# Kernel optimization log

Measured on AMD Instinct MI355X. Metric: run time of the kernel, lower is better.

## Reference

```python
import jax, jax.numpy as jnp
import numpy as np

TOPK, NUM_CLASSES = 13, 80
ALPHA, BETA, GAMMA, EPS = 1.0, 5.0, 3.0, 1e-09


def _make_boxes(key, shape, img=640.0, wmin=10.0, wmax=120.0):
    k1, k2 = jax.random.split(key)
    cxy = jax.random.uniform(k1, shape[:-1] + (2,), minval=0.0, maxval=img)
    wh = jax.random.uniform(k2, shape[:-1] + (2,), minval=wmin, maxval=wmax)
    return jnp.concatenate([cxy - wh / 2, cxy + wh / 2], axis=-1)


def setup_inputs() -> dict:
    key = jax.random.key(0)
    ks = jax.random.split(key, 7)
    bs, A, C, n = 16, 8400, 80, 60
    return {
        'pd_scores': jax.random.uniform(ks[0], (bs, A, C), dtype=jnp.float32),
        'pd_bboxes': _make_boxes(ks[1], (bs, A, 4)),
        'pd_angles': jax.random.uniform(ks[2], (bs, A, 1), minval=0.0, maxval=90.0),
        'anc_points': jax.random.uniform(ks[3], (A, 2), minval=0.0, maxval=640.0),
        'gt_labels': jax.random.randint(ks[4], (bs, n, 1), 0, C, dtype=jnp.int32),
        'gt_bboxes': _make_boxes(ks[5], (bs, n, 4)),
        'gt_angles': jax.random.uniform(ks[6], (bs, n, 1), minval=0.0, maxval=90.0),
        'mask_gt': jnp.ones((bs, n, 1), jnp.float32),
        'epoch_num': 1,
    }


def _cos_fn(x, ar, beta=2.0):
    return 0.5 + 0.5 * jnp.cos(beta / ar * x / 180.0 * jnp.pi + jnp.pi * (1.0 - beta / (2.0 * ar)))


def _angle_measure(pd_angles, gt_angles, gt_bboxes):
    # gt area ratio w/h -> (bs, n, 1, 1)
    w = gt_bboxes[..., 2:3] - gt_bboxes[..., 0:1]
    h = gt_bboxes[..., 3:4] - gt_bboxes[..., 1:2]
    ar = (w / (h + 1e-05))[:, :, None, :]
    theta = jnp.abs(gt_angles[:, :, None, :] - pd_angles[:, None, :, :])  # (bs,n,A,1)
    av = 1.0 / ar / (2.0 - 1.0 / ar)
    mx = _cos_fn(0.0, ar)
    mn = _cos_fn(90.0, ar)
    r = (_cos_fn(theta, ar) - mn) / (mx - mn) * (1.0 - av) + av
    r = jnp.where(jnp.isnan(r), 0.0, r)
    return jnp.squeeze(r, -1)  # (bs, n, A)


def _pairwise_iou(gt, pd):
    # gt (bs,n,4), pd (bs,A,4) -> (bs,n,A)
    lt = jnp.maximum(gt[:, :, None, :2], pd[:, None, :, :2])
    rb = jnp.minimum(gt[:, :, None, 2:], pd[:, None, :, 2:])
    inter = jnp.clip(rb - lt, 0.0).prod(-1)
    a1 = jnp.clip(gt[..., 2:] - gt[..., :2], 0.0).prod(-1)[:, :, None]
    a2 = jnp.clip(pd[..., 2:] - pd[..., :2], 0.0).prod(-1)[:, None, :]
    return inter / (a1 + a2 - inter + EPS)


def _select_topk(metrics, topk_mask):
    bs, n, A = metrics.shape
    _, idxs = jax.lax.top_k(metrics, TOPK)
    idxs = jnp.where(topk_mask, idxs, 0)
    flat = idxs.reshape(bs * n, TOPK)
    cnt = jnp.zeros((bs * n, A), jnp.int32).at[jnp.arange(bs * n)[:, None], flat].add(1)
    cnt = cnt.reshape(bs, n, A)
    return jnp.where(cnt > 1, 0, cnt).astype(metrics.dtype)


def _select_highest_overlaps(mask_pos, overlaps, n):
    fg = mask_pos.sum(-2)                                   # (bs, A)
    multi = fg[:, None, :] > 1                              # (bs, 1, A)
    is_max = jax.nn.one_hot(overlaps.argmax(1), n, axis=1, dtype=mask_pos.dtype)  # (bs,n,A)
    mask_pos = jnp.where(multi, is_max, mask_pos)
    fg = mask_pos.sum(-2)
    tgt_idx = mask_pos.argmax(-2)                           # (bs, A)
    return tgt_idx, fg, mask_pos


def reference(pd_scores, pd_bboxes, pd_angles, anc_points, gt_labels, gt_bboxes, gt_angles, mask_gt, epoch_num):
    bs, A, C = pd_scores.shape
    n = gt_bboxes.shape[1]
    lab = gt_labels[..., 0].astype(jnp.int32)               # (bs, n)

    # bbox_scores: pd_scores[b, :, gt_label] -> (bs, n, A)
    pts = jnp.transpose(pd_scores, (0, 2, 1))               # (bs, C, A)
    bbox_scores = jnp.take_along_axis(pts, lab[:, :, None], axis=1)

    overlaps = _pairwise_iou(gt_bboxes, pd_bboxes)          # (bs, n, A)
    ang = _angle_measure(pd_angles, gt_angles, gt_bboxes)   # (bs, n, A)
    align = bbox_scores ** ALPHA * overlaps ** BETA * ang ** GAMMA

    # anchors-inside-gt mask (bs, n, A)
    lt = anc_points[None, None, :, :] - gt_bboxes[:, :, None, :2]
    rb = gt_bboxes[:, :, None, 2:] - anc_points[None, None, :, :]
    in_gts = (jnp.concatenate([lt, rb], -1).min(-1) > EPS).astype(align.dtype)

    topk_mask = jnp.broadcast_to(mask_gt > 0, (bs, n, TOPK))
    mask_topk = _select_topk(align * in_gts, topk_mask)
    mask_pos = mask_topk * in_gts * mask_gt                 # (bs, n, A)

    tgt_idx, fg, mask_pos = _select_highest_overlaps(mask_pos, overlaps, n)

    # gather per-anchor targets from flattened gt tensors
    off = tgt_idx + jnp.arange(bs, dtype=tgt_idx.dtype)[:, None] * n   # (bs, A)
    tlab = lab.reshape(-1)[off]
    tlab = jnp.where(tlab < 0, 0, tlab)
    tbb = gt_bboxes.reshape(-1, 4)[off]                     # (bs, A, 4)
    tang = gt_angles.reshape(-1, 1)[off]                    # (bs, A, 1)
    ts = jax.nn.one_hot(tlab, C, dtype=pd_scores.dtype)     # (bs, A, C)
    ts = jnp.where(fg[:, :, None] > 0, ts, 0.0)

    # normalized alignment metric scaling
    align = align * mask_pos
    pam = align.max(-1, keepdims=True)                      # (bs, n, 1)
    pov = (overlaps * mask_pos).max(-1, keepdims=True)      # (bs, n, 1)
    norm = (align * pov / (pam + EPS)).max(-2)[:, :, None]  # (bs, A, 1)
    ts = ts * norm

    return tlab, tbb, tang, ts, fg > 0
```

## Files before the change

### kernel.cpp

```cpp
#include <hip/hip_runtime.h>
#include <math.h>

#define TOPK 13
#define PI_F 3.14159265358979323846f
#define RPB 4
#define NC 4
#define CAP 64

typedef unsigned int u32;
typedef unsigned long long u64;

__device__ __forceinline__ u32 ford(float f) {
    u32 u = __float_as_uint(f);
    return (u & 0x80000000u) ? ~u : (u | 0x80000000u);
}
__device__ __forceinline__ float funord(u32 o) {
    u32 u = (o & 0x80000000u) ? (o & 0x7FFFFFFFu) : ~o;
    return __uint_as_float(u);
}

__device__ __forceinline__ float iou_fn(float4 g, float4 p) {
    float ltx = fmaxf(g.x, p.x), lty = fmaxf(g.y, p.y);
    float rbx = fminf(g.z, p.z), rby = fminf(g.w, p.w);
    float inter = fmaxf(rbx - ltx, 0.0f) * fmaxf(rby - lty, 0.0f);
    float a1 = fmaxf(g.z - g.x, 0.0f) * fmaxf(g.w - g.y, 0.0f);
    float a2 = fmaxf(p.z - p.x, 0.0f) * fmaxf(p.w - p.y, 0.0f);
    return inter / (((a1 + a2) - inter) + 1e-9f);
}

struct RowParams { float av, bar, offc, mx, mn; };

__device__ __forceinline__ RowParams row_params(float4 g) {
    float w = g.z - g.x, h = g.w - g.y;
    float ar = w / (h + 1e-5f);
    float ia = 1.0f / ar;
    RowParams rp;
    rp.av = ia / (2.0f - ia);
    rp.bar = 2.0f / ar;
    rp.offc = PI_F * (1.0f - 2.0f / (2.0f * ar));
    rp.mx = 0.5f + 0.5f * cosf(rp.offc);
    rp.mn = 0.5f + 0.5f * cosf(rp.bar * 90.0f / 180.0f * PI_F + rp.offc);
    return rp;
}

__device__ __forceinline__ float ang_measure(const RowParams& rp, float theta) {
    float cfv = 0.5f + 0.5f * cosf(rp.bar * theta / 180.0f * PI_F + rp.offc);
    float r = (cfv - rp.mn) / (rp.mx - rp.mn) * (1.0f - rp.av) + rp.av;
    return isnan(r) ? 0.0f : r;
}

__device__ __forceinline__ float align_fn(float s, float iou, float r) {
    float iou2 = iou * iou;
    float iou5 = (iou2 * iou2) * iou;
    float r3 = (r * r) * r;
    return (s * iou5) * r3;
}

__global__ void k0_init(int* cnt, int* assign1, u32* pam, u32* pov, int BA, int BN) {
    int t = blockIdx.x * blockDim.x + threadIdx.x;
    if (t < BA) { cnt[t] = 0; assign1[t] = -1; }
    if (t < BN) { pam[t] = 0x80000000u; pov[t] = 0x80000000u; }
}

__global__ __launch_bounds__(256)
void k1_topk(const float* __restrict__ scores, const float* __restrict__ pbox,
             const float* __restrict__ pang, const float* __restrict__ anc,
             const int* __restrict__ glab, const float* __restrict__ gbox,
             const float* __restrict__ gang, const float* __restrict__ mgt,
             u64* __restrict__ wslist, float* __restrict__ out,
             int bs, int A, int n, int C) {
    int j = blockIdx.x;
    int b = j % bs;
    int r2 = j / bs;
    int NG = (n + RPB - 1) / RPB;
    int rg = r2 % NG;
    int c0 = r2 / NG;
    int i0 = rg * RPB;
    int tid = threadIdx.x;
    int BA = bs * A;

    int nF4 = BA * (C / 4);
    int zCH = (nF4 + gridDim.x - 1) / gridDim.x;
    int zBeg = j * zCH + tid;
    int zEnd = min(j * zCH + zCH, nF4);
    float4* tsf4 = (float4*)(out + (size_t)BA * 6);
    const float4 z4 = make_float4(0.0f, 0.0f, 0.0f, 0.0f);

    __shared__ u64 posL[RPB][CAP];
    __shared__ u64 zdump[RPB][256];
    __shared__ int pc[RPB];
    if (tid < RPB) pc[tid] = 0;

    float4 g[RPB];
    float rpav[RPB], rpbar[RPB], rpoff[RPB], rpmx[RPB], rpmn[RPB];
    float ga[RPB];
    int lab[RPB];
    bool act[RPB];
#pragma unroll
    for (int r = 0; r < RPB; ++r) {
        int i = i0 + r;
        act[r] = false;
        g[r] = make_float4(0.0f, 0.0f, 0.0f, 0.0f);
        ga[r] = 0.0f; lab[r] = 0;
        rpav[r] = rpbar[r] = rpoff[r] = rpmx[r] = rpmn[r] = 0.0f;
        if (i < n) {
            int bi = b * n + i;
            if (mgt[bi] > 0.0f) {
                act[r] = true;
                g[r] = ((const float4*)gbox)[bi];
                RowParams rp = row_params(g[r]);
                rpav[r] = rp.av; rpbar[r] = rp.bar; rpoff[r] = rp.offc;
                rpmx[r] = rp.mx; rpmn[r] = rp.mn;
                ga[r] = gang[bi];
                lab[r] = glab[bi];
            }
        }
    }
    __syncthreads();

    const float4* pb = ((const float4*)pbox) + (size_t)b * A;
    const float* pa = pang + (size_t)b * A;
    const float2* ac = (const float2*)anc;
    const float* scb = scores + (size_t)b * A * C;

    int CS = (A + NC - 1) / NC;
    int start = c0 * CS;
    int end = min(start + CS, A);
    int clampE = end - 1;

    u64 zkey[RPB];
#pragma unroll
    for (int r = 0; r < RPB; ++r) zkey[r] = 0ull;

    int a = start + tid;
    float4 p = pb[a];
    float pav = pa[a];
    float2 apt = ac[a];

    int nit = (end - start + 255) >> 8;
    for (int it = 0; it < nit; ++it) {
        int an = a + 256;
        int can = min(an, clampE);
        float4 p2 = pb[can];
        float pav2 = pa[can];
        float2 apt2 = ac[can];
        if (zBeg < zEnd) { tsf4[zBeg] = z4; zBeg += 256; }
        if (zBeg < zEnd) { tsf4[zBeg] = z4; zBeg += 256; }
        if (a < end) {
#pragma unroll
            for (int r = 0; r < RPB; ++r) {
                if (!act[r]) continue;
                float mnv = fminf(fminf(apt.x - g[r].x, apt.y - g[r].y),
                                  fminf(g[r].z - apt.x, g[r].w - apt.y));
                float iou = iou_fn(g[r], p);
                bool na = (mnv > 1e-9f) && (iou > 0.0f);
                if (na || zkey[r] == 0ull) {
                    RowParams rp;
                    rp.av = rpav[r]; rp.bar = rpbar[r]; rp.offc = rpoff[r];
                    rp.mx = rpmx[r]; rp.mn = rpmn[r];
                    float th = fabsf(ga[r] - pav);
                    float rr = ang_measure(rp, th);
                    bool zc;
                    if (na && rr > 0.0f) {
                        float s = scb[(size_t)a * C + lab[r]];
                        float v = align_fn(s, iou, rr);
                        if (v > 0.0f) {
                            zc = false;
                            u64 key = ((u64)ford(v) << 32) | (u64)(0xFFFFFFFFu - (u32)a);
                            int idx = atomicAdd(&pc[r], 1);
                            if (idx < CAP) posL[r][idx] = key;
                        } else zc = true;
                    } else zc = (rr >= 0.0f);
                    if (zc && zkey[r] == 0ull)
                        zkey[r] = (0x80000000ull << 32) | (u64)(0xFFFFFFFFu - (u32)a);
                }
            }
        }
        a = an; p = p2; pav = pav2; apt = apt2;
    }
    for (; zBeg < zEnd; zBeg += 256) tsf4[zBeg] = z4;

#pragma unroll
    for (int r = 0; r < RPB; ++r) zdump[r][tid] = zkey[r];
    __syncthreads();

    int lane = tid & 63, wv = tid >> 6;

#define MERGE_ROW(RR)                                                          \
    {                                                                          \
        if (act[RR]) {                                                         \
            u64* dst = wslist + ((size_t)(b * n + i0 + RR) * NC + c0) * TOPK;  \
            int P = pc[RR];                                                    \
            if (P <= CAP) {                                                    \
                u64 s0 = (lane < P) ? posL[RR][lane] : 0ull;                   \
                u64 s1 = zdump[RR][lane];                                      \
                u64 s2 = zdump[RR][lane + 64];                                 \
                u64 s3 = zdump[RR][lane + 128];                                \
                u64 s4 = zdump[RR][lane + 192];                                \
                for (int round = 0; round < TOPK; ++round) {                   \
                    u64 m = s0;                                                \
                    if (s1 > m) m = s1;                                        \
                    if (s2 > m) m = s2;                                        \
                    if (s3 > m) m = s3;                                        \
                    if (s4 > m) m = s4;                                        \
                    for (int st = 32; st > 0; st >>= 1) {                      \
                        u64 o = __shfl_xor(m, st, 64);                         \
                        if (o > m) m = o;                                      \
                    }                                                          \
                    if (lane == 0) dst[round] = m;                             \
                    if (m != 0ull) {                                           \
                        if (s0 == m) s0 = 0ull;                                \
                        else if (s1 == m) s1 = 0ull;                           \
                        else if (s2 == m) s2 = 0ull;                           \
                        else if (s3 == m) s3 = 0ull;                           \
                        else if (s4 == m) s4 = 0ull;                           \
                    }                                                          \
                }                                                              \
            } else {                                                           \
                   \
                u64 last = 0xFFFFFFFFFFFFFFFFull;                              \
                for (int round = 0; round < TOPK; ++round) {                   \
                    u64 best = 0ull;                                           \
                    for (int aa = start + lane; aa < end; aa += 64) {          \
                        float2 ap2 = ac[aa];                                   \
                        float4 pp = pb[aa];                                    \
                        float mnv = fminf(fminf(ap2.x - g[RR].x,               \
                                                ap2.y - g[RR].y),              \
                                          fminf(g[RR].z - ap2.x,               \
                                                g[RR].w - ap2.y));             \
                        float iou = iou_fn(g[RR], pp);                         \
                        bool na = (mnv > 1e-9f) && (iou > 0.0f);               \
                        RowParams rp;                                          \
                        rp.av = rpav[RR]; rp.bar = rpbar[RR];                  \
                        rp.offc = rpoff[RR];                                   \
                        rp.mx = rpmx[RR]; rp.mn = rpmn[RR];                    \
                        float th = fabsf(ga[RR] - pa[aa]);                     \
                        float rr = ang_measure(rp, th);                        \
                        u64 zk = (0x80000000ull << 32) |                       \
                                 (u64)(0xFFFFFFFFu - (u32)aa);                 \
                        u64 key = 0ull;                                        \
                        if (na && rr > 0.0f) {                                 \
                            float s = scb[(size_t)aa * C + lab[RR]];           \
                            float v = align_fn(s, iou, rr);                    \
                            key = (v > 0.0f)                                   \
                                ? (((u64)ford(v) << 32) |                      \
                                   (u64)(0xFFFFFFFFu - (u32)aa))               \
                                : zk;                                          \
                        } else if (rr >= 0.0f) { key = zk; }                   \
                        if (key < last && key > best) best = key;              \
                    }                                                          \
                    u64 m = best;                                              \
                    for (int st = 32; st > 0; st >>= 1) {                      \
                        u64 o = __shfl_xor(m, st, 64);                         \
                        if (o > m) m = o;                                      \
                    }                                                          \
                    if (lane == 0) dst[round] = m;                             \
                    last = m;                                                  \
                }                                                              \
            }                                                                  \
        }                                                                      \
    }

    if (wv == 0) { MERGE_ROW(0) }
    else if (wv == 1) { MERGE_ROW(1) }
    else if (wv == 2) { MERGE_ROW(2) }
    else { MERGE_ROW(3) }
#undef MERGE_ROW
}

__global__ __launch_bounds__(64)
void k1m_merge(const float* __restrict__ anc, const float* __restrict__ gbox,
               const float* __restrict__ mgt, const u64* __restrict__ wslist,
               int* __restrict__ cnt, int* __restrict__ assign1,
               int bs, int A, int n) {
    int j = blockIdx.x;
    int b = j % bs;
    int i = j / bs;
    int bi = b * n + i;
    if (!(mgt[bi] > 0.0f)) return;
    int lane = threadIdx.x;

    const int NK = NC * TOPK;
    const u64* src = wslist + (size_t)bi * NK;
    u64 ka = (lane < NK) ? src[lane] : 0ull;

    float4 g = ((const float4*)gbox)[bi];
    const float2* ac = (const float2*)anc;

    for (int round = 0; round < TOPK; round++) {
        u64 m = ka;
#pragma unroll
        for (int st = 32; st > 0; st >>= 1) {
            u64 o = __shfl_xor(m, st, 64);
            if (o > m) m = o;
        }
        if (m == 0ull) break;
        if (ka == m) {
            ka = 0ull;
            int aa = (int)(0xFFFFFFFFu - (u32)(m & 0xFFFFFFFFull));
            float2 apt = ac[aa];
            float mnv = fminf(fminf(apt.x - g.x, apt.y - g.y),
                              fminf(g.z - apt.x, g.w - apt.y));
            if (mnv > 1e-9f) {
                atomicAdd(&cnt[(size_t)b * A + aa], 1);
                atomicMax(&assign1[(size_t)b * A + aa], i);
            }
        }
    }
}

__global__ __launch_bounds__(256)
void k2_resolve(const float* __restrict__ scores, const float* __restrict__ pbox,
                const float* __restrict__ pang, const int* __restrict__ glab,
                const float* __restrict__ gbox, const float* __restrict__ gang,
                const int* __restrict__ cnt, const int* __restrict__ assign1,
                int* __restrict__ assign, float* __restrict__ alignv,
                u32* __restrict__ pam, u32* __restrict__ pov,
                int bs, int A, int n, int C) {
    int t = blockIdx.x * blockDim.x + threadIdx.x;
    if (t >= bs * A) return;
    int b = t / A;
    int c = cnt[t];
    int asg = -1;
    float alv = 0.0f;
    if (c > 0) {
        float4 p = ((const float4*)pbox)[t];
        if (c == 1) {
            asg = assign1[t];
        } else {
            float best = -1.0f;
            asg = 0;
            for (int i = 0; i < n; i++) {
                float4 gi = ((const float4*)gbox)[b * n + i];
                float io = iou_fn(gi, p);
                if (io > best) { best = io; asg = i; }
            }
        }
        float4 g = ((const float4*)gbox)[b * n + asg];
        RowParams rp = row_params(g);
        float iou = iou_fn(g, p);
        float th = fabsf(gang[b * n + asg] - pang[t]);
        float r = ang_measure(rp, th);
        float s = scores[(size_t)t * C + glab[b * n + asg]];
        alv = align_fn(s, iou, r);
        atomicMax(&pam[b * n + asg], ford(alv));
        atomicMax(&pov[b * n + asg], ford(iou));
    }
    assign[t] = asg;
    alignv[t] = alv;
}

__global__ __launch_bounds__(256)
void k3_out(const int* __restrict__ glab, const float* __restrict__ gbox,
            const float* __restrict__ gang, const int* __restrict__ assign,
            const float* __restrict__ alignv, const u32* __restrict__ pam,
            const u32* __restrict__ pov, float* __restrict__ out,
            int bs, int A, int n, int C) {
    int t = blockIdx.x * blockDim.x + threadIdx.x;
    int BA = bs * A;
    if (t >= BA) return;
    int b = t / A;
    int asg = assign[t];
    bool fg = asg >= 0;
    int tgt = fg ? asg : 0;
    int lb = glab[b * n + tgt];
    if (lb < 0) lb = 0;

    out[t] = (float)lb;
    ((float4*)(out + BA))[t] = ((const float4*)gbox)[b * n + tgt];
    out[(size_t)BA * 5 + t] = gang[b * n + tgt];
    out[(size_t)BA * 6 + (size_t)BA * C + t] = fg ? 1.0f : 0.0f;

    if (fg) {
        float pamv = funord(pam[b * n + asg]);
        float povv = funord(pov[b * n + asg]);
        float vv = (alignv[t] * povv) / (pamv + 1e-9f);
        out[(size_t)BA * 6 + (size_t)t * C + lb] = fmaxf(vv, 0.0f);
    }
}

extern "C" void kernel_launch(void* const* d_in, const int* in_sizes, int n_in,
                              void* d_out, int out_size, void* d_ws, size_t ws_size,
                              hipStream_t stream) {
    const float* scores = (const float*)d_in[0];
    const float* pbox = (const float*)d_in[1];
    const float* pang = (const float*)d_in[2];
    const float* anc = (const float*)d_in[3];
    const int* glab = (const int*)d_in[4];
    const float* gbox = (const float*)d_in[5];
    const float* gang = (const float*)d_in[6];
    const float* mgt = (const float*)d_in[7];

    const int C = 80;
    int A = in_sizes[3] / 2;
    int bs = in_sizes[0] / (A * C);
    int n = in_sizes[4] / bs;
    int BA = bs * A;
    int BN = bs * n;

    char* ws = (char*)d_ws;
    u64* wslist = (u64*)ws;     ws += sizeof(u64) * (size_t)BN * NC * TOPK;
    int* cnt = (int*)ws;        ws += sizeof(int) * (size_t)BA;
    int* assign1 = (int*)ws;    ws += sizeof(int) * (size_t)BA;
    int* assign = (int*)ws;     ws += sizeof(int) * (size_t)BA;
    float* alignv = (float*)ws; ws += sizeof(float) * (size_t)BA;
    u32* pam = (u32*)ws;        ws += sizeof(u32) * (size_t)BN;
    u32* pov = (u32*)ws;        ws += sizeof(u32) * (size_t)BN;

    int NG = (n + RPB - 1) / RPB;

    k0_init<<<(BA + 255) / 256, 256, 0, stream>>>(cnt, assign1, pam, pov, BA, BN);
    k1_topk<<<bs * NG * NC, 256, 0, stream>>>(scores, pbox, pang, anc, glab, gbox, gang,
                                              mgt, wslist, (float*)d_out, bs, A, n, C);
    k1m_merge<<<BN, 64, 0, stream>>>(anc, gbox, mgt, wslist, cnt, assign1, bs, A, n);
    k2_resolve<<<(BA + 255) / 256, 256, 0, stream>>>(scores, pbox, pang, glab, gbox, gang,
                                                     cnt, assign1, assign, alignv, pam, pov,
                                                     bs, A, n, C);
    k3_out<<<(BA + 255) / 256, 256, 0, stream>>>(glab, gbox, gang, assign, alignv, pam, pov,
                                                 (float*)d_out, bs, A, n, C);
}
```

Measured before the change: 173.8 us.

## Fuse per-row top-k merge into top-k kernel via last-block-done counter

Removes the separate k1m_merge launch. Each chunk block now publishes its partial top-k with atomic exchanges and bumps a per-row completion counter. The last chunk to finish for a row merges the candidates and does the cnt/assign1 atomics. This saves one kernel launch and the gap between launches, at the cost of extra fences, atomics and a serialized merge inside the top-k kernel.

```diff
diff --git a/kernel.cpp b/kernel.cpp
--- a/kernel.cpp
+++ b/kernel.cpp
@@ -56,10 +56,11 @@
     return (s * iou5) * r3;
 }
 
-__global__ void k0_init(int* cnt, int* assign1, u32* pam, u32* pov, int BA, int BN) {
+__global__ void k0_init(int* cnt, int* assign1, u32* pam, u32* pov, int* rowdone,
+                        int BA, int BN) {
     int t = blockIdx.x * blockDim.x + threadIdx.x;
     if (t < BA) { cnt[t] = 0; assign1[t] = -1; }
-    if (t < BN) { pam[t] = 0x80000000u; pov[t] = 0x80000000u; }
+    if (t < BN) { pam[t] = 0x80000000u; pov[t] = 0x80000000u; rowdone[t] = 0; }
 }
 
 __global__ __launch_bounds__(256)
@@ -67,7 +68,9 @@
              const float* __restrict__ pang, const float* __restrict__ anc,
              const int* __restrict__ glab, const float* __restrict__ gbox,
              const float* __restrict__ gang, const float* __restrict__ mgt,
-             u64* __restrict__ wslist, float* __restrict__ out,
+             u64* __restrict__ wslist, int* __restrict__ rowdone,
+             int* __restrict__ cnt, int* __restrict__ assign1,
+             float* __restrict__ out,
              int bs, int A, int n, int C) {
     int j = blockIdx.x;
     int b = j % bs;
@@ -189,7 +192,8 @@
 #define MERGE_ROW(RR)                                                          \
     {                                                                          \
         if (act[RR]) {                                                         \
-            u64* dst = wslist + ((size_t)(b * n + i0 + RR) * NC + c0) * TOPK;  \
+            int bi_r = b * n + i0 + RR;                                        \
+            u64* dst = wslist + ((size_t)bi_r * NC + c0) * TOPK;               \
             int P = pc[RR];                                                    \
             if (P <= CAP) {                                                    \
                 u64 s0 = (lane < P) ? posL[RR][lane] : 0ull;                   \
@@ -207,7 +211,7 @@
                         u64 o = __shfl_xor(m, st, 64);                         \
                         if (o > m) m = o;                                      \
                     }                                                          \
-                    if (lane == 0) dst[round] = m;                             \
+                    if (lane == 0) atomicExch(&dst[round], m);                 \
                     if (m != 0ull) {                                           \
                         if (s0 == m) s0 = 0ull;                                \
                         else if (s1 == m) s1 = 0ull;                           \
@@ -254,8 +258,43 @@
                         u64 o = __shfl_xor(m, st, 64);                         \
                         if (o > m) m = o;                                      \
                     }                                                          \
-                    if (lane == 0) dst[round] = m;                             \
+                    if (lane == 0) atomicExch(&dst[round], m);                 \
                     last = m;                                                  \
+                }                                                              \
+            }                                                                  \
+                \
+            int old = 0;                                                       \
+            if (lane == 0) {                                                   \
+                __threadfence();                                               \
+                old = atomicAdd(&rowdone[bi_r], 1);                            \
+            }                                                                  \
+            old = __shfl(old, 0, 64);                                          \
+            if (old == NC - 1) {                                               \
+                __threadfence();                                  \
+                u64* src = wslist + (size_t)bi_r * (NC * TOPK);                \
+                u64 ka = (lane < NC * TOPK)                                    \
+                       ? atomicAdd(&src[lane], 0ull) : 0ull;                   \
+                for (int round = 0; round < TOPK; ++round) {                   \
+                    u64 m = ka;                                                \
+                    for (int st = 32; st > 0; st >>= 1) {                      \
+                        u64 o = __shfl_xor(m, st, 64);                         \
+                        if (o > m) m = o;                                      \
+                    }                                                          \
+                    if (m == 0ull) break;             \
+                    if (ka == m) {                      \
+                        ka = 0ull;                                             \
+                        int aa = (int)(0xFFFFFFFFu -                           \
+                                       (u32)(m & 0xFFFFFFFFull));              \
+                        float2 ap2 = ac[aa];                                   \
+                        float mnw = fminf(fminf(ap2.x - g[RR].x,               \
+                                                ap2.y - g[RR].y),              \
+                                          fminf(g[RR].z - ap2.x,               \
+                                                g[RR].w - ap2.y));             \
+                        if (mnw > 1e-9f) {                                     \
+                            atomicAdd(&cnt[(size_t)b * A + aa], 1);            \
+                            atomicMax(&assign1[(size_t)b * A + aa], i0 + RR);  \
+                        }                                                      \
+                    }                                                          \
                 }                                                              \
             }                                                                  \
         }                                                                      \
@@ -266,47 +305,6 @@
     else if (wv == 2) { MERGE_ROW(2) }
     else { MERGE_ROW(3) }
 #undef MERGE_ROW
-}
-
-__global__ __launch_bounds__(64)
-void k1m_merge(const float* __restrict__ anc, const float* __restrict__ gbox,
-               const float* __restrict__ mgt, const u64* __restrict__ wslist,
-               int* __restrict__ cnt, int* __restrict__ assign1,
-               int bs, int A, int n) {
-    int j = blockIdx.x;
-    int b = j % bs;
-    int i = j / bs;
-    int bi = b * n + i;
-    if (!(mgt[bi] > 0.0f)) return;
-    int lane = threadIdx.x;
-
-    const int NK = NC * TOPK;
-    const u64* src = wslist + (size_t)bi * NK;
-    u64 ka = (lane < NK) ? src[lane] : 0ull;
-
-    float4 g = ((const float4*)gbox)[bi];
-    const float2* ac = (const float2*)anc;
-
-    for (int round = 0; round < TOPK; round++) {
-        u64 m = ka;
-#pragma unroll
-        for (int st = 32; st > 0; st >>= 1) {
-            u64 o = __shfl_xor(m, st, 64);
-            if (o > m) m = o;
-        }
-        if (m == 0ull) break;
-        if (ka == m) {
-            ka = 0ull;
-            int aa = (int)(0xFFFFFFFFu - (u32)(m & 0xFFFFFFFFull));
-            float2 apt = ac[aa];
-            float mnv = fminf(fminf(apt.x - g.x, apt.y - g.y),
-                              fminf(g.z - apt.x, g.w - apt.y));
-            if (mnv > 1e-9f) {
-                atomicAdd(&cnt[(size_t)b * A + aa], 1);
-                atomicMax(&assign1[(size_t)b * A + aa], i);
-            }
-        }
-    }
 }
 
 __global__ __launch_bounds__(256)
@@ -406,13 +404,14 @@
     float* alignv = (float*)ws; ws += sizeof(float) * (size_t)BA;
     u32* pam = (u32*)ws;        ws += sizeof(u32) * (size_t)BN;
     u32* pov = (u32*)ws;        ws += sizeof(u32) * (size_t)BN;
+    int* rowdone = (int*)ws;    ws += sizeof(int) * (size_t)BN;
 
     int NG = (n + RPB - 1) / RPB;
 
-    k0_init<<<(BA + 255) / 256, 256, 0, stream>>>(cnt, assign1, pam, pov, BA, BN);
+    k0_init<<<(BA + 255) / 256, 256, 0, stream>>>(cnt, assign1, pam, pov, rowdone, BA, BN);
     k1_topk<<<bs * NG * NC, 256, 0, stream>>>(scores, pbox, pang, anc, glab, gbox, gang,
-                                              mgt, wslist, (float*)d_out, bs, A, n, C);
-    k1m_merge<<<BN, 64, 0, stream>>>(anc, gbox, mgt, wslist, cnt, assign1, bs, A, n);
+                                              mgt, wslist, rowdone, cnt, assign1,
+                                              (float*)d_out, bs, A, n, C);
     k2_resolve<<<(BA + 255) / 256, 256, 0, stream>>>(scores, pbox, pang, glab, gbox, gang,
                                                      cnt, assign1, assign, alignv, pam, pov,
                                                      bs, A, n, C);
```

Measured after the change: 239.7 us. 37.9% more time.
